# Kernel optimization log

Hardware: AMD Instinct MI355X
Metric: run time of the kernel (lower is better)

The kernel has to match this reference:

```python
import jax, jax.numpy as jnp
import numpy as np

BN_EPS = 1e-5


def setup_inputs() -> dict:
    key = jax.random.key(0)
    ks = jax.random.split(key, 6)
    b, c_out, c_high = 8, 256, 512
    h1 = w1 = 64
    h2 = w2 = 32
    return {
        "fms_low": jax.random.normal(ks[0], (b, c_out, h1, w1), jnp.float32),
        "fms_high": jax.random.normal(ks[1], (b, c_high, h2, w2), jnp.float32),
        "w_conv": jax.random.normal(ks[2], (c_out, c_high), jnp.float32) * (1.0 / np.sqrt(c_high)),
        "bn_gamma": jnp.ones((c_out,), jnp.float32),
        "bn_beta": jnp.zeros((c_out,), jnp.float32),
        "bn_mean": jnp.zeros((c_out,), jnp.float32),
        "bn_var": jnp.ones((c_out,), jnp.float32),
        "fc1_w": jax.random.normal(ks[3], (c_out // 4, c_out), jnp.float32) * (1.0 / np.sqrt(c_out)),
        "fc1_b": jnp.zeros((c_out // 4,), jnp.float32),
        "fc2_w": jax.random.normal(ks[4], (c_out // 4, c_out), jnp.float32) * (1.0 / np.sqrt(c_out)),
        "fc2_b": jnp.zeros((c_out // 4,), jnp.float32),
        "scale": jax.random.normal(ks[5], (1,), jnp.float32),
    }


def reference(fms_low, fms_high, w_conv, bn_gamma, bn_beta, bn_mean, bn_var,
              fc1_w, fc1_b, fc2_w, fc2_b, scale):
    b, c, h1, w1 = fms_low.shape
    # conv_high: 1x1 conv (no bias) + BN (inference) + ReLU
    x = jnp.einsum('bchw,oc->bohw', fms_high, w_conv)  # [b, 256, h2, w2]
    inv = bn_gamma / jnp.sqrt(bn_var + BN_EPS)
    x = x * inv[None, :, None, None] + (bn_beta - bn_mean * inv)[None, :, None, None]
    x = jax.nn.relu(x)
    # raw row-major reshapes, matching torch .view(b, -1, C)
    feat_low = fms_low.reshape(b, -1, c)    # [b, N_low, 256]
    feat_high = x.reshape(b, -1, c)         # [b, N_high, 256]
    mid_low = feat_low @ fc1_w.T + fc1_b    # [b, N_low, 64]
    mid_high = feat_high @ fc2_w.T + fc2_b  # [b, N_high, 64]
    energy = jnp.einsum('bnd,bmd->bnm', mid_low, mid_high)  # [b, N_low, N_high]
    attn = jax.nn.softmax(energy, axis=-1)
    # bmm(feat_high^T, attn^T) -> [b, 256, N_low]
    mid = jnp.einsum('bmc,bnm->bcn', feat_high, attn).reshape(b, c, h1, w1)
    return scale[0] * mid
```

## Files before the change

kernel.cpp:

```cpp
#include <hip/hip_runtime.h>
#include <hip/hip_bf16.h>

typedef __bf16 v8bf __attribute__((ext_vector_type(8)));
typedef float  v4f  __attribute__((ext_vector_type(4)));

typedef __attribute__((address_space(3))) void       lds_vd;
typedef __attribute__((address_space(1))) const void gbl_vd;

#define MFMA16(a, b, c) __builtin_amdgcn_mfma_f32_16x16x32_bf16(a, b, c, 0, 0, 0)

__device__ __forceinline__ void split_hl(float v, __bf16* h, __bf16* l) {
    __bf16 hh = (__bf16)v;
    *h = hh;
    *l = (__bf16)(v - (float)hh);
}

__device__ __forceinline__ int swz_idx(int row, int col) {
    return row * 64 + ((((col >> 3) ^ (row & 7))) << 3) + (col & 7);
}
__device__ __forceinline__ const __bf16* frag_ptr(const __bf16* base, int row, int g) {
    return base + row * 64 + ((g ^ (row & 7)) << 3);
}


__global__ __launch_bounds__(256) void k_conv(
    const float* __restrict__ FH, const float* __restrict__ W,
    const float* __restrict__ gamma, const float* __restrict__ beta,
    const float* __restrict__ mean, const float* __restrict__ var,
    __bf16* __restrict__ Xhi, __bf16* __restrict__ Xlo, __bf16* __restrict__ VT)
{
    __shared__ __align__(16) __bf16 Ah[64 * 64];
    __shared__ __align__(16) __bf16 Al[64 * 64];
    __shared__ __align__(16) __bf16 Bh[64 * 64];
    __shared__ __align__(16) __bf16 Bl[64 * 64];
    __shared__ float invl[64], shl[64];

    const int tid = threadIdx.x, lane = tid & 63, w = tid >> 6;
    const int l15 = lane & 15, quad = lane >> 4;
    const int u0 = blockIdx.x * 16, o0 = blockIdx.y * 64, b = blockIdx.z;
    const float* FHb = FH + (size_t)b * 524288;

    if (tid < 64) {
        const int o = o0 + tid;
        const float iv = gamma[o] * rsqrtf(var[o] + 1e-5f);
        invl[tid] = iv;
        shl[tid] = beta[o] - mean[o] * iv;
    }

    const int ao = tid >> 2, aseg = tid & 3;
    float wreg[16], freg[16];
    {
        const float* wp = W + (size_t)(o0 + ao) * 512 + aseg * 16;
        #pragma unroll
        for (int q = 0; q < 4; ++q) {
            float4 f = ((const float4*)wp)[q];
            wreg[4*q] = f.x; wreg[4*q+1] = f.y; wreg[4*q+2] = f.z; wreg[4*q+3] = f.w;
        }
        const float* fp = FHb + (size_t)lane * 1024 + w * 256 + u0;
        #pragma unroll
        for (int q = 0; q < 4; ++q) {
            float4 f = ((const float4*)fp)[q];
            freg[4*q] = f.x; freg[4*q+1] = f.y; freg[4*q+2] = f.z; freg[4*q+3] = f.w;
        }
    }

    v4f acc[2][2];
    #pragma unroll
    for (int i = 0; i < 2; ++i)
        #pragma unroll
        for (int j = 0; j < 2; ++j) { v4f z = {0.f,0.f,0.f,0.f}; acc[i][j] = z; }
    const int oh = w >> 1, nh = w & 1;

    for (int ch = 0; ch < 8; ++ch) {
        if (ch) __syncthreads();
        #pragma unroll
        for (int z = 0; z < 2; ++z) {
            v8bf hv, lv;
            #pragma unroll
            for (int e = 0; e < 8; ++e) {
                __bf16 h, l; split_hl(wreg[8*z + e], &h, &l);
                hv[e] = h; lv[e] = l;
            }
            const int gi = (2*aseg + z) ^ (ao & 7);
            *(v8bf*)(Ah + ao*64 + (gi << 3)) = hv;
            *(v8bf*)(Al + ao*64 + (gi << 3)) = lv;
        }
        #pragma unroll
        for (int ul = 0; ul < 16; ++ul) {
            __bf16 h, l; split_hl(freg[ul], &h, &l);
            const int idx = (w*16 + ul)*64 + (((lane >> 3) ^ (ul & 7)) << 3) + (lane & 7);
            Bh[idx] = h; Bl[idx] = l;
        }
        __syncthreads();
        if (ch < 7) {
            const int c1 = (ch + 1) * 64;
            const float* wp = W + (size_t)(o0 + ao) * 512 + c1 + aseg * 16;
            #pragma unroll
            for (int q = 0; q < 4; ++q) {
                float4 f = ((const float4*)wp)[q];
                wreg[4*q] = f.x; wreg[4*q+1] = f.y; wreg[4*q+2] = f.z; wreg[4*q+3] = f.w;
            }
            const float* fp = FHb + (size_t)(c1 + lane) * 1024 + w * 256 + u0;
            #pragma unroll
            for (int q = 0; q < 4; ++q) {
                float4 f = ((const float4*)fp)[q];
                freg[4*q] = f.x; freg[4*q+1] = f.y; freg[4*q+2] = f.z; freg[4*q+3] = f.w;
            }
        }
        #pragma unroll
        for (int ks = 0; ks < 2; ++ks) {
            const int g = 4*ks + quad;
            v8bf a_h[2], a_l[2], b_h[2], b_l[2];
            #pragma unroll
            for (int i = 0; i < 2; ++i) {
                const int row = oh*32 + i*16 + l15;
                a_h[i] = *(const v8bf*)frag_ptr(Ah, row, g);
                a_l[i] = *(const v8bf*)frag_ptr(Al, row, g);
            }
            #pragma unroll
            for (int j = 0; j < 2; ++j) {
                const int row = nh*32 + j*16 + l15;
                b_h[j] = *(const v8bf*)frag_ptr(Bh, row, g);
                b_l[j] = *(const v8bf*)frag_ptr(Bl, row, g);
            }
            #pragma unroll
            for (int i = 0; i < 2; ++i)
                #pragma unroll
                for (int j = 0; j < 2; ++j) {
                    acc[i][j] = MFMA16(a_h[i], b_h[j], acc[i][j]);
                    acc[i][j] = MFMA16(a_h[i], b_l[j], acc[i][j]);
                    acc[i][j] = MFMA16(a_l[i], b_h[j], acc[i][j]);
                }
        }
    }
    __syncthreads();

    #pragma unroll
    for (int i = 0; i < 2; ++i)
        #pragma unroll
        for (int j = 0; j < 2; ++j)
            #pragma unroll
            for (int r = 0; r < 4; ++r) {
                const int row = oh*32 + i*16 + quad*4 + r;
                const int col = nh*32 + j*16 + l15;
                float v = acc[i][j][r] * invl[row] + shl[row];
                v = fmaxf(v, 0.f);
                __bf16 h, l; split_hl(v, &h, &l);
                const int idx = swz_idx(row, col);
                Ah[idx] = h; Al[idx] = l;
            }
    __syncthreads();
    {
        const int o = tid >> 2, pv = tid & 3;
        const size_t gbase = ((size_t)b*256 + o0 + o) * 1024 + pv*256 + u0;
        #pragma unroll
        for (int z = 0; z < 2; ++z) {
            const int gi = (2*pv + z) ^ (o & 7);
            v8bf h = *(v8bf*)(Ah + o*64 + (gi << 3));
            v8bf l = *(v8bf*)(Al + o*64 + (gi << 3));
            *(v8bf*)(Xhi + gbase + z*8) = h;
            *(v8bf*)(Xlo + gbase + z*8) = l;
        }
    }
    {
        const int ul = tid >> 4, s = tid & 15;
        __bf16 tmp[16];
        #pragma unroll
        for (int k = 0; k < 16; ++k) {
            const int m = s*16 + k;
            const int row = m >> 2;
            const int col = (m & 3)*16 + ul;
            tmp[k] = Ah[swz_idx(row, col)];
        }
        __bf16* vp = VT + ((size_t)b*256 + u0 + ul) * 1024 + 4*o0 + s*16;
        *(v8bf*)(vp)     = *(v8bf*)(tmp);
        *(v8bf*)(vp + 8) = *(v8bf*)(tmp + 8);
    }
}

__global__ __launch_bounds__(256) void k_proj32(
    const float* __restrict__ Feat, const float* __restrict__ Wfc,
    const float* __restrict__ bfc,
    __bf16* __restrict__ Ohi, __bf16* __restrict__ Olo)
{
    __shared__ __align__(16) __bf16 Bh[64 * 256];
    __shared__ __align__(16) __bf16 Bl[64 * 256];
    __shared__ __align__(16) __bf16 Eo[4][16 * 64];

    const int tid = threadIdx.x, lane = tid & 63, w = tid >> 6;
    const int l15 = lane & 15, quad = lane >> 4;
    const int r0 = blockIdx.x * 64;
    const int row = r0 + w*16 + l15;

    const float* ap = Feat + (size_t)row * 256 + quad * 8;
    float acur[8], anxt[8];
    {
        float4 f0 = ((const float4*)ap)[0];
        float4 f1 = ((const float4*)ap)[1];
        acur[0]=f0.x; acur[1]=f0.y; acur[2]=f0.z; acur[3]=f0.w;
        acur[4]=f1.x; acur[5]=f1.y; acur[6]=f1.z; acur[7]=f1.w;
    }

    {
        const int n = tid >> 2, q4 = tid & 3, n7 = n & 7;
        const float* wp = Wfc + (size_t)n * 256 + q4 * 64;
        #pragma unroll
        for (int z = 0; z < 8; ++z) {
            float4 f0 = ((const float4*)wp)[2*z];
            float4 f1 = ((const float4*)wp)[2*z + 1];
            float w8[8] = {f0.x, f0.y, f0.z, f0.w, f1.x, f1.y, f1.z, f1.w};
            v8bf hv, lv;
            #pragma unroll
            for (int e = 0; e < 8; ++e) {
                __bf16 h, l; split_hl(w8[e], &h, &l);
                hv[e] = h; lv[e] = l;
            }
            const int gsw = (q4*8 + z) ^ n7;
            *(v8bf*)(Bh + n*256 + gsw*8) = hv;
            *(v8bf*)(Bl + n*256 + gsw*8) = lv;
        }
    }
    __syncthreads();

    v4f acc[4];
    #pragma unroll
    for (int j = 0; j < 4; ++j) { v4f z = {0.f,0.f,0.f,0.f}; acc[j] = z; }

    const int l7 = l15 & 7;
    const __bf16* bh_base = Bh + l15*256;
    const __bf16* bl_base = Bl + l15*256;

    #pragma unroll
    for (int kc = 0; kc < 8; ++kc) {
        if (kc < 7) {
            float4 f0 = ((const float4*)(ap + (kc+1)*32))[0];
            float4 f1 = ((const float4*)(ap + (kc+1)*32))[1];
            anxt[0]=f0.x; anxt[1]=f0.y; anxt[2]=f0.z; anxt[3]=f0.w;
            anxt[4]=f1.x; anxt[5]=f1.y; anxt[6]=f1.z; anxt[7]=f1.w;
        }
        v8bf ah, al;
        #pragma unroll
        for (int e = 0; e < 8; ++e) {
            __bf16 h, l; split_hl(acur[e], &h, &l);
            ah[e] = h; al[e] = l;
        }
        const int goff = (((kc*4 + quad) ^ l7) << 3);
        #pragma unroll
        for (int j = 0; j < 4; ++j) {
            v8bf bh = *(const v8bf*)(bh_base + j*4096 + goff);
            v8bf bl = *(const v8bf*)(bl_base + j*4096 + goff);
            acc[j] = MFMA16(ah, bh, acc[j]);
            acc[j] = MFMA16(ah, bl, acc[j]);
            acc[j] = MFMA16(al, bh, acc[j]);
        }
        #pragma unroll
        for (int e = 0; e < 8; ++e) acur[e] = anxt[e];
    }

    __bf16* eo = &Eo[w][0];
    __bf16 lb[4][4];
    #pragma unroll
    for (int j = 0; j < 4; ++j) {
        const float bias = bfc[j*16 + l15];
        #pragma unroll
        for (int r = 0; r < 4; ++r) {
            __bf16 h, l; split_hl(acc[j][r] + bias, &h, &l);
            lb[j][r] = l;
            eo[swz_idx(quad*4 + r, j*16 + l15)] = h;
        }
    }
    const size_t orow = (size_t)row * 64;
    #pragma unroll
    for (int z = 0; z < 2; ++z) {
        const int gi = (2*quad + z) ^ l7;
        *(v8bf*)(Ohi + orow + quad*16 + z*8) = *(v8bf*)(eo + l15*64 + gi*8);
    }
    #pragma unroll
    for (int j = 0; j < 4; ++j)
        #pragma unroll
        for (int r = 0; r < 4; ++r)
            eo[swz_idx(quad*4 + r, j*16 + l15)] = lb[j][r];
    #pragma unroll
    for (int z = 0; z < 2; ++z) {
        const int gi = (2*quad + z) ^ l7;
        *(v8bf*)(Olo + orow + quad*16 + z*8) = *(v8bf*)(eo + l15*64 + gi*8);
    }
}

__global__ __launch_bounds__(256) void k_projbf(
    const __bf16* __restrict__ Fhi, const __bf16* __restrict__ Flo,
    const float* __restrict__ Wfc, const float* __restrict__ bfc,
    __bf16* __restrict__ Ohi, __bf16* __restrict__ Olo)
{
    __shared__ __align__(16) __bf16 Bh[64 * 256];
    __shared__ __align__(16) __bf16 Bl[64 * 256];
    __shared__ __align__(16) __bf16 Eo[4][16 * 64];

    const int tid = threadIdx.x, lane = tid & 63, w = tid >> 6;
    const int l15 = lane & 15, quad = lane >> 4;
    const int r0 = blockIdx.x * 64;
    const int row = r0 + w*16 + l15;

    const __bf16* fh = Fhi + (size_t)row * 256 + quad * 8;
    const __bf16* fl = Flo + (size_t)row * 256 + quad * 8;
    v8bf ah = *(const v8bf*)(fh);
    v8bf al = *(const v8bf*)(fl);

    {
        const int n = tid >> 2, q4 = tid & 3, n7 = n & 7;
        const float* wp = Wfc + (size_t)n * 256 + q4 * 64;
        #pragma unroll
        for (int z = 0; z < 8; ++z) {
            float4 f0 = ((const float4*)wp)[2*z];
            float4 f1 = ((const float4*)wp)[2*z + 1];
            float w8[8] = {f0.x, f0.y, f0.z, f0.w, f1.x, f1.y, f1.z, f1.w};
            v8bf hv, lv;
            #pragma unroll
            for (int e = 0; e < 8; ++e) {
                __bf16 h, l; split_hl(w8[e], &h, &l);
                hv[e] = h; lv[e] = l;
            }
            const int gsw = (q4*8 + z) ^ n7;
            *(v8bf*)(Bh + n*256 + gsw*8) = hv;
            *(v8bf*)(Bl + n*256 + gsw*8) = lv;
        }
    }
    __syncthreads();

    v4f acc[4];
    #pragma unroll
    for (int j = 0; j < 4; ++j) { v4f z = {0.f,0.f,0.f,0.f}; acc[j] = z; }

    const int l7 = l15 & 7;
    const __bf16* bh_base = Bh + l15*256;
    const __bf16* bl_base = Bl + l15*256;

    #pragma unroll
    for (int kc = 0; kc < 8; ++kc) {
        v8bf anh, anl;
        if (kc < 7) {
            anh = *(const v8bf*)(fh + (kc+1)*32);
            anl = *(const v8bf*)(fl + (kc+1)*32);
        }
        const int goff = (((kc*4 + quad) ^ l7) << 3);
        #pragma unroll
        for (int j = 0; j < 4; ++j) {
            v8bf bh = *(const v8bf*)(bh_base + j*4096 + goff);
            v8bf bl = *(const v8bf*)(bl_base + j*4096 + goff);
            acc[j] = MFMA16(ah, bh, acc[j]);
            acc[j] = MFMA16(ah, bl, acc[j]);
            acc[j] = MFMA16(al, bh, acc[j]);
        }
        if (kc < 7) { ah = anh; al = anl; }
    }

    __bf16* eo = &Eo[w][0];
    __bf16 lb[4][4];
    #pragma unroll
    for (int j = 0; j < 4; ++j) {
        const float bias = bfc[j*16 + l15];
        #pragma unroll
        for (int r = 0; r < 4; ++r) {
            __bf16 h, l; split_hl(acc[j][r] + bias, &h, &l);
            lb[j][r] = l;
            eo[swz_idx(quad*4 + r, j*16 + l15)] = h;
        }
    }
    const size_t orow = (size_t)row * 64;
    #pragma unroll
    for (int z = 0; z < 2; ++z) {
        const int gi = (2*quad + z) ^ l7;
        *(v8bf*)(Ohi + orow + quad*16 + z*8) = *(v8bf*)(eo + l15*64 + gi*8);
    }
    #pragma unroll
    for (int j = 0; j < 4; ++j)
        #pragma unroll
        for (int r = 0; r < 4; ++r)
            eo[swz_idx(quad*4 + r, j*16 + l15)] = lb[j][r];
    #pragma unroll
    for (int z = 0; z < 2; ++z) {
        const int gi = (2*quad + z) ^ l7;
        *(v8bf*)(Olo + orow + quad*16 + z*8) = *(v8bf*)(eo + l15*64 + gi*8);
    }
}

__global__ __launch_bounds__(512, 4) void k_attn(
    const __bf16* __restrict__ MLhi, const __bf16* __restrict__ MLlo,
    const __bf16* __restrict__ MHhi, const __bf16* __restrict__ MHlo,
    const __bf16* __restrict__ VT,
    const float* __restrict__ scale_p,
    float* __restrict__ out)
{
    __shared__ __align__(16) __bf16 Khi[2][32 * 64];
    __shared__ __align__(16) __bf16 Klo[2][32 * 64];
    __shared__ __align__(16) __bf16 Vs [2][256 * 32];
    __shared__ __align__(16) __bf16 Ps [2][4][16 * 32];
    __shared__ float lsh[2][4][16];

    const int tid = threadIdx.x, lane = tid & 63, w = tid >> 6;
    const int l15 = lane & 15, quad = lane >> 4;
    const int b = blockIdx.x & 7, qtb = blockIdx.x >> 3;
    const int q0 = qtb * 64;
    const int qt = w & 3, mb = w >> 2;

    v8bf qhi[2], qlo[2];
    {
        const __bf16* qp  = MLhi + ((size_t)(b*4096 + q0 + qt*16 + l15)) * 64;
        const __bf16* qlp = MLlo + ((size_t)(b*4096 + q0 + qt*16 + l15)) * 64;
        #pragma unroll
        for (int h = 0; h < 2; ++h) {
            qhi[h] = *(const v8bf*)(qp + h*32 + quad*8);
            qlo[h] = *(const v8bf*)(qlp + h*32 + quad*8);
        }
    }
    #pragma unroll
    for (int h = 0; h < 2; ++h) {
        asm volatile("" : "+v"(qhi[h]));
        asm volatile("" : "+v"(qlo[h]));
    }

    const char* Khg = (const char*)(MHhi + (size_t)b * 65536);
    const char* Klg = (const char*)(MHlo + (size_t)b * 65536);
    const char* Vg  = (const char*)(VT + (size_t)b * 262144);
    const int offK = (lane >> 3) * 128 + (((lane & 7) ^ ((lane >> 3) & 7)) << 4);
    const int offV = (lane >> 2) * 2048 + ((((lane & 3) ^ ((lane >> 3) & 3))) << 4);

    const char* kgsrc = (w < 4) ? Khg : Klg;
    const int ksub = (w & 3) * 1024;

    v4f oacc[4][2];
    #pragma unroll
    for (int t = 0; t < 4; ++t)
        #pragma unroll
        for (int cb = 0; cb < 2; ++cb) { v4f z = {0.f,0.f,0.f,0.f}; oacc[t][cb] = z; }
    float lrow[4] = {0.f, 0.f, 0.f, 0.f};

    {
        char* kdst = (char*)((w < 4) ? &Khi[0][0] : &Klo[0][0]);
        __builtin_amdgcn_global_load_lds((gbl_vd*)(kgsrc + ksub + offK),
                                         (lds_vd*)(kdst + ksub), 16, 0, 0);
        #pragma unroll
        for (int j = 0; j < 2; ++j) {
            const int i = w*2 + j;
            __builtin_amdgcn_global_load_lds((gbl_vd*)(Vg + i*32768 + offV),
                                             (lds_vd*)((char*)&Vs[0][0] + i*1024), 16, 0, 0);
        }
    }
    asm volatile("s_waitcnt vmcnt(2)\n\ts_barrier" ::: "memory");

    for (int ch = 0; ch < 32; ++ch) {
        const int cur = ch & 1, nxt = cur ^ 1;
        const int mn = ((ch < 31) ? (ch + 1) : 31) * 32;

        {
            char* kdst = (char*)((w < 4) ? &Khi[nxt][0] : &Klo[nxt][0]);
            __builtin_amdgcn_global_load_lds((gbl_vd*)(kgsrc + mn*128 + ksub + offK),
                                             (lds_vd*)(kdst + ksub), 16, 0, 0);
        }

        v4f sacc = {0.f, 0.f, 0.f, 0.f};
        __builtin_amdgcn_s_setprio(1);
        #pragma unroll
        for (int h = 0; h < 2; ++h) {
            const int row = mb*16 + l15, g = 4*h + quad;
            v8bf kh = *(const v8bf*)frag_ptr(&Khi[cur][0], row, g);
            v8bf kl = *(const v8bf*)frag_ptr(&Klo[cur][0], row, g);
            sacc = MFMA16(qhi[h], kh, sacc);
            sacc = MFMA16(qhi[h], kl, sacc);
            sacc = MFMA16(qlo[h], kh, sacc);
        }
        __builtin_amdgcn_s_setprio(0);

        #pragma unroll
        for (int r = 0; r < 4; ++r) {
            const float p = __expf(sacc[r]);
            lrow[r] += p;
            const int row = quad*4 + r;
            const int slot = (mb*2 + (l15 >> 3)) ^ ((row >> 1) & 3);
            Ps[cur][qt][row*32 + (slot << 3) + (l15 & 7)] = (__bf16)p;
        }

        if (ch) {
            const int pb = nxt;
            v8bf pa[4];
            #pragma unroll
            for (int t = 0; t < 4; ++t)
                pa[t] = *(const v8bf*)(&Ps[pb][t][0] + l15*32 + ((quad ^ ((l15 >> 1) & 3)) << 3));
            __builtin_amdgcn_s_setprio(1);
            #pragma unroll
            for (int cb = 0; cb < 2; ++cb) {
                const int vrow = w*32 + cb*16 + l15;
                v8bf vv = *(const v8bf*)(&Vs[pb][0] + vrow*32 + ((quad ^ ((vrow >> 1) & 3)) << 3));
                #pragma unroll
                for (int t = 0; t < 4; ++t)
                    oacc[t][cb] = MFMA16(pa[t], vv, oacc[t][cb]);
            }
            __builtin_amdgcn_s_setprio(0);
        }

        asm volatile("s_waitcnt lgkmcnt(0)" ::: "memory");
        #pragma unroll
        for (int j = 0; j < 2; ++j) {
            const int i = w*2 + j;
            __builtin_amdgcn_global_load_lds((gbl_vd*)(Vg + mn*2 + i*32768 + offV),
                                             (lds_vd*)((char*)&Vs[nxt][0] + i*1024), 16, 0, 0);
        }

        asm volatile("s_waitcnt vmcnt(2) lgkmcnt(0)\n\ts_barrier" ::: "memory");
    }

    {
        v8bf pa[4];
        #pragma unroll
        for (int t = 0; t < 4; ++t)
            pa[t] = *(const v8bf*)(&Ps[1][t][0] + l15*32 + ((quad ^ ((l15 >> 1) & 3)) << 3));
        #pragma unroll
        for (int cb = 0; cb < 2; ++cb) {
            const int vrow = w*32 + cb*16 + l15;
            v8bf vv = *(const v8bf*)(&Vs[1][0] + vrow*32 + ((quad ^ ((vrow >> 1) & 3)) << 3));
            #pragma unroll
            for (int t = 0; t < 4; ++t)
                oacc[t][cb] = MFMA16(pa[t], vv, oacc[t][cb]);
        }
    }

    #pragma unroll
    for (int r = 0; r < 4; ++r) {
        float s = lrow[r];
        #pragma unroll
        for (int d = 1; d < 16; d <<= 1) s += __shfl_xor(s, d, 64);
        lrow[r] = s;
    }
    if (l15 == 0) {
        #pragma unroll
        for (int r = 0; r < 4; ++r) lsh[mb][qt][quad*4 + r] = lrow[r];
    }
    __syncthreads();

    const float scl = scale_p[0];
    float inv[4][4];
    #pragma unroll
    for (int t = 0; t < 4; ++t)
        #pragma unroll
        for (int r = 0; r < 4; ++r)
            inv[t][r] = scl / (lsh[0][t][quad*4 + r] + lsh[1][t][quad*4 + r]);
    float* outb = out + (size_t)b * 256 * 4096;
    #pragma unroll
    for (int cb = 0; cb < 2; ++cb) {
        const int c = w*32 + cb*16 + l15;
        #pragma unroll
        for (int t = 0; t < 4; ++t) {
            float4 v;
            v.x = oacc[t][cb][0] * inv[t][0];
            v.y = oacc[t][cb][1] * inv[t][1];
            v.z = oacc[t][cb][2] * inv[t][2];
            v.w = oacc[t][cb][3] * inv[t][3];
            *(float4*)(outb + (size_t)c * 4096 + q0 + t*16 + quad*4) = v;
        }
    }
}

extern "C" void kernel_launch(void* const* d_in, const int* in_sizes, int n_in,
                              void* d_out, int out_size, void* d_ws, size_t ws_size,
                              hipStream_t stream)
{
    const float* fms_low  = (const float*)d_in[0];
    const float* fms_high = (const float*)d_in[1];
    const float* w_conv   = (const float*)d_in[2];
    const float* gamma    = (const float*)d_in[3];
    const float* beta     = (const float*)d_in[4];
    const float* mean     = (const float*)d_in[5];
    const float* var      = (const float*)d_in[6];
    const float* fc1_w    = (const float*)d_in[7];
    const float* fc1_b    = (const float*)d_in[8];
    const float* fc2_w    = (const float*)d_in[9];
    const float* fc2_b    = (const float*)d_in[10];
    const float* scale    = (const float*)d_in[11];
    float* out = (float*)d_out;

    __bf16* Xhi  = (__bf16*)d_ws;
    __bf16* Xlo  = Xhi  + (size_t)8*256*1024;
    __bf16* VT   = Xlo  + (size_t)8*256*1024;
    __bf16* MLhi = VT   + (size_t)8*256*1024;
    __bf16* MLlo = MLhi + (size_t)8*4096*64;
    __bf16* MHhi = MLlo + (size_t)8*4096*64;
    __bf16* MHlo = MHhi + (size_t)8*1024*64;

    k_conv<<<dim3(16, 4, 8), 256, 0, stream>>>(fms_high, w_conv, gamma, beta,
                                               mean, var, Xhi, Xlo, VT);
    k_projbf<<<dim3(128), 256, 0, stream>>>(Xhi, Xlo, fc2_w, fc2_b, MHhi, MHlo);
    k_proj32<<<dim3(512), 256, 0, stream>>>(fms_low, fc1_w, fc1_b, MLhi, MLlo);
    k_attn<<<dim3(512), 512, 0, stream>>>(MLhi, MLlo, MHhi, MHlo, VT, scale, out);
}
```

Before: 184.8 us.

## Pre-split conv inputs to bf16 and double-buffer conv tiles via direct LDS loads

Adds a pre-pass kernel that converts the high-level feature map (transposed) and the conv weights into bf16 hi/lo pairs in workspace. The conv kernel then streams these pre-split tiles into double-buffered shared memory with global_load_lds, overlapping the next chunk's load with the current MFMA work and dropping the in-loop splitting. The cost is an extra kernel launch and extra global traffic for writing and re-reading the split copies.

```diff
diff --git a/kernel.cpp b/kernel.cpp
--- a/kernel.cpp
+++ b/kernel.cpp
@@ -2,6 +2,7 @@
 #include <hip/hip_bf16.h>
 
 typedef __bf16 v8bf __attribute__((ext_vector_type(8)));
+typedef __bf16 v4bf __attribute__((ext_vector_type(4)));
 typedef float  v4f  __attribute__((ext_vector_type(4)));
 
 typedef __attribute__((address_space(3))) void       lds_vd;
@@ -23,22 +24,74 @@
 }
 
 
+__global__ __launch_bounds__(256) void k_pre(
+    const float* __restrict__ FH, const float* __restrict__ W,
+    __bf16* __restrict__ FThi, __bf16* __restrict__ FTlo,
+    __bf16* __restrict__ Whi, __bf16* __restrict__ Wlo)
+{
+    const int blk = blockIdx.x, t = threadIdx.x;
+    if (blk < 1024) {
+        __shared__ __bf16 Th[64][72], Tl[64][72];
+        const int bb = blk >> 7, rem = blk & 127;
+        const int k0 = (rem >> 4) * 64, u0 = (rem & 15) * 64;
+        const float* src = FH + (size_t)bb * 524288 + (size_t)k0 * 1024 + u0;
+        {
+            const int kl = t >> 2, uq = t & 3;
+            const float* sp = src + (size_t)kl * 1024 + uq * 16;
+            #pragma unroll
+            for (int q = 0; q < 4; ++q) {
+                float4 f = ((const float4*)sp)[q];
+                float v[4] = {f.x, f.y, f.z, f.w};
+                #pragma unroll
+                for (int e = 0; e < 4; ++e) {
+                    __bf16 h, l; split_hl(v[e], &h, &l);
+                    const int ul = uq * 16 + q * 4 + e;
+                    Th[ul][kl] = h; Tl[ul][kl] = l;
+                }
+            }
+        }
+        __syncthreads();
+        {
+            const int ul = t >> 2, ks = t & 3;
+            const size_t dof = ((size_t)bb * 1024 + u0 + ul) * 512 + k0 + ks * 16;
+            *(v8bf*)(FThi + dof)     = *(const v8bf*)&Th[ul][ks * 16];
+            *(v8bf*)(FThi + dof + 8) = *(const v8bf*)&Th[ul][ks * 16 + 8];
+            *(v8bf*)(FTlo + dof)     = *(const v8bf*)&Tl[ul][ks * 16];
+            *(v8bf*)(FTlo + dof + 8) = *(const v8bf*)&Tl[ul][ks * 16 + 8];
+        }
+    } else {
+        const int base = (blk - 1024) * 16384 + t * 4;
+        #pragma unroll
+        for (int it = 0; it < 16; ++it) {
+            const int idx = base + it * 1024;
+            float4 f = *(const float4*)(W + idx);
+            float v[4] = {f.x, f.y, f.z, f.w};
+            v4bf hv, lv;
+            #pragma unroll
+            for (int e = 0; e < 4; ++e) {
+                __bf16 h, l; split_hl(v[e], &h, &l);
+                hv[e] = h; lv[e] = l;
+            }
+            *(v4bf*)(Whi + idx) = hv;
+            *(v4bf*)(Wlo + idx) = lv;
+        }
+    }
+}
+
 __global__ __launch_bounds__(256) void k_conv(
-    const float* __restrict__ FH, const float* __restrict__ W,
+    const __bf16* __restrict__ FThi, const __bf16* __restrict__ FTlo,
+    const __bf16* __restrict__ Whi_g, const __bf16* __restrict__ Wlo_g,
     const float* __restrict__ gamma, const float* __restrict__ beta,
     const float* __restrict__ mean, const float* __restrict__ var,
     __bf16* __restrict__ Xhi, __bf16* __restrict__ Xlo, __bf16* __restrict__ VT)
 {
-    __shared__ __align__(16) __bf16 Ah[64 * 64];
-    __shared__ __align__(16) __bf16 Al[64 * 64];
-    __shared__ __align__(16) __bf16 Bh[64 * 64];
-    __shared__ __align__(16) __bf16 Bl[64 * 64];
+    __shared__ __align__(16) __bf16 Wh[2][4096], Wl[2][4096];
+    __shared__ __align__(16) __bf16 Fh[2][4096], Fl[2][4096];
     __shared__ float invl[64], shl[64];
 
     const int tid = threadIdx.x, lane = tid & 63, w = tid >> 6;
     const int l15 = lane & 15, quad = lane >> 4;
     const int u0 = blockIdx.x * 16, o0 = blockIdx.y * 64, b = blockIdx.z;
-    const float* FHb = FH + (size_t)b * 524288;
 
     if (tid < 64) {
         const int o = o0 + tid;
@@ -47,22 +100,32 @@
         shl[tid] = beta[o] - mean[o] * iv;
     }
 
-    const int ao = tid >> 2, aseg = tid & 3;
-    float wreg[16], freg[16];
-    {
-        const float* wp = W + (size_t)(o0 + ao) * 512 + aseg * 16;
-        #pragma unroll
-        for (int q = 0; q < 4; ++q) {
-            float4 f = ((const float4*)wp)[q];
-            wreg[4*q] = f.x; wreg[4*q+1] = f.y; wreg[4*q+2] = f.z; wreg[4*q+3] = f.w;
-        }
-        const float* fp = FHb + (size_t)lane * 1024 + w * 256 + u0;
-        #pragma unroll
-        for (int q = 0; q < 4; ++q) {
-            float4 f = ((const float4*)fp)[q];
-            freg[4*q] = f.x; freg[4*q+1] = f.y; freg[4*q+2] = f.z; freg[4*q+3] = f.w;
-        }
-    }
+    const int r8 = lane >> 3;
+    const int swz16 = ((lane & 7) ^ r8) << 4;
+
+    const char* gsW = (w == 0) ? (const char*)Whi_g : (const char*)Wlo_g;
+    const char* gsF = ((w == 2) ? (const char*)FThi : (const char*)FTlo)
+                      + (size_t)b * 1048576;
+
+    auto STAGE = [&](int buf, int kc) {
+        if (w < 2) {
+            char* ds = (char*)((w == 0) ? &Wh[buf][0] : &Wl[buf][0]);
+            #pragma unroll
+            for (int i = 0; i < 8; ++i)
+                __builtin_amdgcn_global_load_lds(
+                    (gbl_vd*)(gsW + (size_t)(o0 + i*8 + r8) * 1024 + kc*128 + swz16),
+                    (lds_vd*)(ds + i * 1024), 16, 0, 0);
+        } else {
+            char* ds = (char*)((w == 2) ? &Fh[buf][0] : &Fl[buf][0]);
+            #pragma unroll
+            for (int i = 0; i < 8; ++i) {
+                const int w4 = i >> 1, sub = i & 1;
+                __builtin_amdgcn_global_load_lds(
+                    (gbl_vd*)(gsF + (size_t)(w4*256 + u0 + sub*8 + r8) * 1024 + kc*128 + swz16),
+                    (lds_vd*)(ds + i * 1024), 16, 0, 0);
+            }
+        }
+    };
 
     v4f acc[2][2];
     #pragma unroll
@@ -71,42 +134,12 @@
         for (int j = 0; j < 2; ++j) { v4f z = {0.f,0.f,0.f,0.f}; acc[i][j] = z; }
     const int oh = w >> 1, nh = w & 1;
 
+    STAGE(0, 0);
+    __syncthreads();
+
     for (int ch = 0; ch < 8; ++ch) {
-        if (ch) __syncthreads();
-        #pragma unroll
-        for (int z = 0; z < 2; ++z) {
-            v8bf hv, lv;
-            #pragma unroll
-            for (int e = 0; e < 8; ++e) {
-                __bf16 h, l; split_hl(wreg[8*z + e], &h, &l);
-                hv[e] = h; lv[e] = l;
-            }
-            const int gi = (2*aseg + z) ^ (ao & 7);
-            *(v8bf*)(Ah + ao*64 + (gi << 3)) = hv;
-            *(v8bf*)(Al + ao*64 + (gi << 3)) = lv;
-        }
-        #pragma unroll
-        for (int ul = 0; ul < 16; ++ul) {
-            __bf16 h, l; split_hl(freg[ul], &h, &l);
-            const int idx = (w*16 + ul)*64 + (((lane >> 3) ^ (ul & 7)) << 3) + (lane & 7);
-            Bh[idx] = h; Bl[idx] = l;
-        }
-        __syncthreads();
-        if (ch < 7) {
-            const int c1 = (ch + 1) * 64;
-            const float* wp = W + (size_t)(o0 + ao) * 512 + c1 + aseg * 16;
-            #pragma unroll
-            for (int q = 0; q < 4; ++q) {
-                float4 f = ((const float4*)wp)[q];
-                wreg[4*q] = f.x; wreg[4*q+1] = f.y; wreg[4*q+2] = f.z; wreg[4*q+3] = f.w;
-            }
-            const float* fp = FHb + (size_t)(c1 + lane) * 1024 + w * 256 + u0;
-            #pragma unroll
-            for (int q = 0; q < 4; ++q) {
-                float4 f = ((const float4*)fp)[q];
-                freg[4*q] = f.x; freg[4*q+1] = f.y; freg[4*q+2] = f.z; freg[4*q+3] = f.w;
-            }
-        }
+        const int cur = ch & 1;
+        if (ch < 7) STAGE(cur ^ 1, ch + 1);
         #pragma unroll
         for (int ks = 0; ks < 2; ++ks) {
             const int g = 4*ks + quad;
@@ -114,14 +147,14 @@
             #pragma unroll
             for (int i = 0; i < 2; ++i) {
                 const int row = oh*32 + i*16 + l15;
-                a_h[i] = *(const v8bf*)frag_ptr(Ah, row, g);
-                a_l[i] = *(const v8bf*)frag_ptr(Al, row, g);
+                a_h[i] = *(const v8bf*)frag_ptr(&Wh[cur][0], row, g);
+                a_l[i] = *(const v8bf*)frag_ptr(&Wl[cur][0], row, g);
             }
             #pragma unroll
             for (int j = 0; j < 2; ++j) {
                 const int row = nh*32 + j*16 + l15;
-                b_h[j] = *(const v8bf*)frag_ptr(Bh, row, g);
-                b_l[j] = *(const v8bf*)frag_ptr(Bl, row, g);
+                b_h[j] = *(const v8bf*)frag_ptr(&Fh[cur][0], row, g);
+                b_l[j] = *(const v8bf*)frag_ptr(&Fl[cur][0], row, g);
             }
             #pragma unroll
             for (int i = 0; i < 2; ++i)
@@ -132,9 +165,11 @@
                     acc[i][j] = MFMA16(a_l[i], b_h[j], acc[i][j]);
                 }
         }
-    }
-    __syncthreads();
-
+        __syncthreads();
+    }
+
+    __bf16* Ah = &Wh[0][0];
+    __bf16* Al = &Wl[0][0];
     #pragma unroll
     for (int i = 0; i < 2; ++i)
         #pragma unroll
@@ -585,8 +620,13 @@
     __bf16* MLlo = MLhi + (size_t)8*4096*64;
     __bf16* MHhi = MLlo + (size_t)8*4096*64;
     __bf16* MHlo = MHhi + (size_t)8*1024*64;
-
-    k_conv<<<dim3(16, 4, 8), 256, 0, stream>>>(fms_high, w_conv, gamma, beta,
+    __bf16* FThi = MHlo + (size_t)8*1024*64;
+    __bf16* FTlo = FThi + (size_t)8*1024*512;
+    __bf16* Whi  = FTlo + (size_t)8*1024*512;
+    __bf16* Wlo  = Whi  + (size_t)256*512;
+
+    k_pre<<<dim3(1032), 256, 0, stream>>>(fms_high, w_conv, FThi, FTlo, Whi, Wlo);
+    k_conv<<<dim3(16, 4, 8), 256, 0, stream>>>(FThi, FTlo, Whi, Wlo, gamma, beta,
                                                mean, var, Xhi, Xlo, VT);
     k_projbf<<<dim3(128), 256, 0, stream>>>(Xhi, Xlo, fc2_w, fc2_b, MHhi, MHlo);
     k_proj32<<<dim3(512), 256, 0, stream>>>(fms_low, fc1_w, fc1_b, MLhi, MLlo);
```

After: 186.5 us. About the same (+0.9%).

## Merge two projection kernels into one launch and split QK MFMA accumulator chains

Applied to the files above, without the earlier changes.

The two fc projection kernels (fp32 low features and bf16 hi/lo high features) are merged into a single 640-block launch that picks its weights, inputs and outputs by block index. This removes one kernel launch and lets the 128 high-projection blocks run alongside the 512 low ones instead of serializing. Separately, the attention QK score computation now uses two independent accumulators interleaved, so the dependent MFMA chain is shortened, at the cost of one extra vector add and a few more registers.

```diff
diff --git a/kernel.cpp b/kernel.cpp
--- a/kernel.cpp
+++ b/kernel.cpp
@@ -178,10 +178,13 @@
     }
 }
 
-__global__ __launch_bounds__(256) void k_proj32(
-    const float* __restrict__ Feat, const float* __restrict__ Wfc,
-    const float* __restrict__ bfc,
-    __bf16* __restrict__ Ohi, __bf16* __restrict__ Olo)
+__global__ __launch_bounds__(256) void k_proj(
+    const float* __restrict__ Feat,
+    const __bf16* __restrict__ Fhi, const __bf16* __restrict__ Flo,
+    const float* __restrict__ W1, const float* __restrict__ b1,
+    const float* __restrict__ W2, const float* __restrict__ b2,
+    __bf16* __restrict__ O1hi, __bf16* __restrict__ O1lo,
+    __bf16* __restrict__ O2hi, __bf16* __restrict__ O2lo)
 {
     __shared__ __align__(16) __bf16 Bh[64 * 256];
     __shared__ __align__(16) __bf16 Bl[64 * 256];
@@ -189,17 +192,14 @@
 
     const int tid = threadIdx.x, lane = tid & 63, w = tid >> 6;
     const int l15 = lane & 15, quad = lane >> 4;
-    const int r0 = blockIdx.x * 64;
+    const bool low = blockIdx.x < 512;
+    const int r0 = (low ? blockIdx.x : (blockIdx.x - 512)) * 64;
     const int row = r0 + w*16 + l15;
 
-    const float* ap = Feat + (size_t)row * 256 + quad * 8;
-    float acur[8], anxt[8];
-    {
-        float4 f0 = ((const float4*)ap)[0];
-        float4 f1 = ((const float4*)ap)[1];
-        acur[0]=f0.x; acur[1]=f0.y; acur[2]=f0.z; acur[3]=f0.w;
-        acur[4]=f1.x; acur[5]=f1.y; acur[6]=f1.z; acur[7]=f1.w;
-    }
+    const float* Wfc = low ? W1 : W2;
+    const float* bfc = low ? b1 : b2;
+    __bf16* Ohi = low ? O1hi : O2hi;
+    __bf16* Olo = low ? O1lo : O2lo;
 
     {
         const int n = tid >> 2, q4 = tid & 3, n7 = n & 7;
@@ -230,128 +230,64 @@
     const __bf16* bh_base = Bh + l15*256;
     const __bf16* bl_base = Bl + l15*256;
 
-    #pragma unroll
-    for (int kc = 0; kc < 8; ++kc) {
-        if (kc < 7) {
-            float4 f0 = ((const float4*)(ap + (kc+1)*32))[0];
-            float4 f1 = ((const float4*)(ap + (kc+1)*32))[1];
-            anxt[0]=f0.x; anxt[1]=f0.y; anxt[2]=f0.z; anxt[3]=f0.w;
-            anxt[4]=f1.x; anxt[5]=f1.y; anxt[6]=f1.z; anxt[7]=f1.w;
-        }
-        v8bf ah, al;
-        #pragma unroll
-        for (int e = 0; e < 8; ++e) {
-            __bf16 h, l; split_hl(acur[e], &h, &l);
-            ah[e] = h; al[e] = l;
-        }
-        const int goff = (((kc*4 + quad) ^ l7) << 3);
-        #pragma unroll
-        for (int j = 0; j < 4; ++j) {
-            v8bf bh = *(const v8bf*)(bh_base + j*4096 + goff);
-            v8bf bl = *(const v8bf*)(bl_base + j*4096 + goff);
-            acc[j] = MFMA16(ah, bh, acc[j]);
-            acc[j] = MFMA16(ah, bl, acc[j]);
-            acc[j] = MFMA16(al, bh, acc[j]);
-        }
-        #pragma unroll
-        for (int e = 0; e < 8; ++e) acur[e] = anxt[e];
-    }
-
-    __bf16* eo = &Eo[w][0];
-    __bf16 lb[4][4];
-    #pragma unroll
-    for (int j = 0; j < 4; ++j) {
-        const float bias = bfc[j*16 + l15];
-        #pragma unroll
-        for (int r = 0; r < 4; ++r) {
-            __bf16 h, l; split_hl(acc[j][r] + bias, &h, &l);
-            lb[j][r] = l;
-            eo[swz_idx(quad*4 + r, j*16 + l15)] = h;
-        }
-    }
-    const size_t orow = (size_t)row * 64;
-    #pragma unroll
-    for (int z = 0; z < 2; ++z) {
-        const int gi = (2*quad + z) ^ l7;
-        *(v8bf*)(Ohi + orow + quad*16 + z*8) = *(v8bf*)(eo + l15*64 + gi*8);
-    }
-    #pragma unroll
-    for (int j = 0; j < 4; ++j)
-        #pragma unroll
-        for (int r = 0; r < 4; ++r)
-            eo[swz_idx(quad*4 + r, j*16 + l15)] = lb[j][r];
-    #pragma unroll
-    for (int z = 0; z < 2; ++z) {
-        const int gi = (2*quad + z) ^ l7;
-        *(v8bf*)(Olo + orow + quad*16 + z*8) = *(v8bf*)(eo + l15*64 + gi*8);
-    }
-}
-
-__global__ __launch_bounds__(256) void k_projbf(
-    const __bf16* __restrict__ Fhi, const __bf16* __restrict__ Flo,
-    const float* __restrict__ Wfc, const float* __restrict__ bfc,
-    __bf16* __restrict__ Ohi, __bf16* __restrict__ Olo)
-{
-    __shared__ __align__(16) __bf16 Bh[64 * 256];
-    __shared__ __align__(16) __bf16 Bl[64 * 256];
-    __shared__ __align__(16) __bf16 Eo[4][16 * 64];
-
-    const int tid = threadIdx.x, lane = tid & 63, w = tid >> 6;
-    const int l15 = lane & 15, quad = lane >> 4;
-    const int r0 = blockIdx.x * 64;
-    const int row = r0 + w*16 + l15;
-
-    const __bf16* fh = Fhi + (size_t)row * 256 + quad * 8;
-    const __bf16* fl = Flo + (size_t)row * 256 + quad * 8;
-    v8bf ah = *(const v8bf*)(fh);
-    v8bf al = *(const v8bf*)(fl);
-
-    {
-        const int n = tid >> 2, q4 = tid & 3, n7 = n & 7;
-        const float* wp = Wfc + (size_t)n * 256 + q4 * 64;
-        #pragma unroll
-        for (int z = 0; z < 8; ++z) {
-            float4 f0 = ((const float4*)wp)[2*z];
-            float4 f1 = ((const float4*)wp)[2*z + 1];
-            float w8[8] = {f0.x, f0.y, f0.z, f0.w, f1.x, f1.y, f1.z, f1.w};
-            v8bf hv, lv;
+    if (low) {
+        const float* ap = Feat + (size_t)row * 256 + quad * 8;
+        float acur[8], anxt[8];
+        {
+            float4 f0 = ((const float4*)ap)[0];
+            float4 f1 = ((const float4*)ap)[1];
+            acur[0]=f0.x; acur[1]=f0.y; acur[2]=f0.z; acur[3]=f0.w;
+            acur[4]=f1.x; acur[5]=f1.y; acur[6]=f1.z; acur[7]=f1.w;
+        }
+        #pragma unroll
+        for (int kc = 0; kc < 8; ++kc) {
+            if (kc < 7) {
+                float4 f0 = ((const float4*)(ap + (kc+1)*32))[0];
+                float4 f1 = ((const float4*)(ap + (kc+1)*32))[1];
+                anxt[0]=f0.x; anxt[1]=f0.y; anxt[2]=f0.z; anxt[3]=f0.w;
+                anxt[4]=f1.x; anxt[5]=f1.y; anxt[6]=f1.z; anxt[7]=f1.w;
+            }
+            v8bf ah, al;
             #pragma unroll
             for (int e = 0; e < 8; ++e) {
-                __bf16 h, l; split_hl(w8[e], &h, &l);
-                hv[e] = h; lv[e] = l;
-            }
-            const int gsw = (q4*8 + z) ^ n7;
-            *(v8bf*)(Bh + n*256 + gsw*8) = hv;
-            *(v8bf*)(Bl + n*256 + gsw*8) = lv;
-        }
-    }
-    __syncthreads();
-
-    v4f acc[4];
-    #pragma unroll
-    for (int j = 0; j < 4; ++j) { v4f z = {0.f,0.f,0.f,0.f}; acc[j] = z; }
-
-    const int l7 = l15 & 7;
-    const __bf16* bh_base = Bh + l15*256;
-    const __bf16* bl_base = Bl + l15*256;
-
-    #pragma unroll
-    for (int kc = 0; kc < 8; ++kc) {
-        v8bf anh, anl;
-        if (kc < 7) {
-            anh = *(const v8bf*)(fh + (kc+1)*32);
-            anl = *(const v8bf*)(fl + (kc+1)*32);
-        }
-        const int goff = (((kc*4 + quad) ^ l7) << 3);
-        #pragma unroll
-        for (int j = 0; j < 4; ++j) {
-            v8bf bh = *(const v8bf*)(bh_base + j*4096 + goff);
-            v8bf bl = *(const v8bf*)(bl_base + j*4096 + goff);
-            acc[j] = MFMA16(ah, bh, acc[j]);
-            acc[j] = MFMA16(ah, bl, acc[j]);
-            acc[j] = MFMA16(al, bh, acc[j]);
-        }
-        if (kc < 7) { ah = anh; al = anl; }
+                __bf16 h, l; split_hl(acur[e], &h, &l);
+                ah[e] = h; al[e] = l;
+            }
+            const int goff = (((kc*4 + quad) ^ l7) << 3);
+            #pragma unroll
+            for (int j = 0; j < 4; ++j) {
+                v8bf bh = *(const v8bf*)(bh_base + j*4096 + goff);
+                v8bf bl = *(const v8bf*)(bl_base + j*4096 + goff);
+                acc[j] = MFMA16(ah, bh, acc[j]);
+                acc[j] = MFMA16(ah, bl, acc[j]);
+                acc[j] = MFMA16(al, bh, acc[j]);
+            }
+            #pragma unroll
+            for (int e = 0; e < 8; ++e) acur[e] = anxt[e];
+        }
+    } else {
+        const __bf16* fh = Fhi + (size_t)row * 256 + quad * 8;
+        const __bf16* fl = Flo + (size_t)row * 256 + quad * 8;
+        v8bf ah = *(const v8bf*)(fh);
+        v8bf al = *(const v8bf*)(fl);
+        #pragma unroll
+        for (int kc = 0; kc < 8; ++kc) {
+            v8bf anh, anl;
+            if (kc < 7) {
+                anh = *(const v8bf*)(fh + (kc+1)*32);
+                anl = *(const v8bf*)(fl + (kc+1)*32);
+            }
+            const int goff = (((kc*4 + quad) ^ l7) << 3);
+            #pragma unroll
+            for (int j = 0; j < 4; ++j) {
+                v8bf bh = *(const v8bf*)(bh_base + j*4096 + goff);
+                v8bf bl = *(const v8bf*)(bl_base + j*4096 + goff);
+                acc[j] = MFMA16(ah, bh, acc[j]);
+                acc[j] = MFMA16(ah, bl, acc[j]);
+                acc[j] = MFMA16(al, bh, acc[j]);
+            }
+            if (kc < 7) { ah = anh; al = anl; }
+        }
     }
 
     __bf16* eo = &Eo[w][0];
@@ -458,18 +394,23 @@
                                              (lds_vd*)(kdst + ksub), 16, 0, 0);
         }
 
-        v4f sacc = {0.f, 0.f, 0.f, 0.f};
+        v4f s0 = {0.f, 0.f, 0.f, 0.f}, s1 = {0.f, 0.f, 0.f, 0.f};
         __builtin_amdgcn_s_setprio(1);
-        #pragma unroll
-        for (int h = 0; h < 2; ++h) {
-            const int row = mb*16 + l15, g = 4*h + quad;
-            v8bf kh = *(const v8bf*)frag_ptr(&Khi[cur][0], row, g);
-            v8bf kl = *(const v8bf*)frag_ptr(&Klo[cur][0], row, g);
-            sacc = MFMA16(qhi[h], kh, sacc);
-            sacc = MFMA16(qhi[h], kl, sacc);
-            sacc = MFMA16(qlo[h], kh, sacc);
+        {
+            const int row = mb*16 + l15;
+            v8bf kh0 = *(const v8bf*)frag_ptr(&Khi[cur][0], row, quad);
+            v8bf kl0 = *(const v8bf*)frag_ptr(&Klo[cur][0], row, quad);
+            v8bf kh1 = *(const v8bf*)frag_ptr(&Khi[cur][0], row, 4 + quad);
+            v8bf kl1 = *(const v8bf*)frag_ptr(&Klo[cur][0], row, 4 + quad);
+            s0 = MFMA16(qhi[0], kh0, s0);
+            s1 = MFMA16(qhi[1], kh1, s1);
+            s0 = MFMA16(qhi[0], kl0, s0);
+            s1 = MFMA16(qhi[1], kl1, s1);
+            s0 = MFMA16(qlo[0], kh0, s0);
+            s1 = MFMA16(qlo[1], kh1, s1);
         }
         __builtin_amdgcn_s_setprio(0);
+        v4f sacc = s0 + s1;
 
         #pragma unroll
         for (int r = 0; r < 4; ++r) {
@@ -588,7 +529,8 @@
 
     k_conv<<<dim3(16, 4, 8), 256, 0, stream>>>(fms_high, w_conv, gamma, beta,
                                                mean, var, Xhi, Xlo, VT);
-    k_projbf<<<dim3(128), 256, 0, stream>>>(Xhi, Xlo, fc2_w, fc2_b, MHhi, MHlo);
-    k_proj32<<<dim3(512), 256, 0, stream>>>(fms_low, fc1_w, fc1_b, MLhi, MLlo);
+    k_proj<<<dim3(640), 256, 0, stream>>>(fms_low, Xhi, Xlo,
+                                          fc1_w, fc1_b, fc2_w, fc2_b,
+                                          MLhi, MLlo, MHhi, MHlo);
     k_attn<<<dim3(512), 512, 0, stream>>>(MLhi, MLlo, MHhi, MHlo, VT, scale, out);
 }
```

After: 180.8 us. 1.02x faster.
